# Optimization experiments

Measured on AMD Instinct MI355X. Metric: run time of the kernel, lower is better.

Reference implementation:

```python
import jax, jax.numpy as jnp
import numpy as np
from jax import lax

T = 8192          # in_length
D = 128           # embed_dim
SIGMA_MIN = 0.4
SIGMA_MAX = 3.0
NOISE_SIGMA = 0.01
GAUSS_C = 0.39894228  # 1/sqrt(2*pi), as hardcoded in the source


def setup_inputs() -> dict:
    key = jax.random.key(0)
    kx, kn = jax.random.split(key)
    X = jax.random.uniform(kx, (1, T), dtype=jnp.float32)            # spike train: X > 0.5 fires
    weight = jnp.ones((1, D), dtype=jnp.float32)                      # module buffer: ones -> uniform softmax
    noise = NOISE_SIGMA * jax.random.normal(kn, (1, T), dtype=jnp.float32)
    sigma = jnp.linspace(SIGMA_MIN, SIGMA_MAX, D, dtype=jnp.float32)  # kernel widths
    return {"X": X, "weight": weight, "noise": noise, "sigma": sigma}


def reference(X, weight, noise, sigma):
    Tlen = X.shape[1]
    # Gaussian kernel bank, exactly as Gaussian_kernel_fix: peak at index j == T
    j = jnp.arange(2 * Tlen - 1, dtype=X.dtype)
    d2 = (j - Tlen) ** 2                                              # [2T-1]
    K = (GAUSS_C / sigma)[:, None] * jnp.exp(-d2[None, :] / (2.0 * sigma * sigma)[:, None])  # [D, 2T-1]

    # GKE: embed[d, t] = sum_i 1{X[0,i] > 0.5} * K[d, T-1 + t - i]  == full convolution, 'same' slice
    spikes = (X > 0.5).astype(X.dtype)                                # [1, T]
    Kf = K[:, ::-1][:, None, :]                                       # flip -> lax cross-correlation computes the conv; [D, 1, 2T-1]
    embed = lax.conv_general_dilated(
        spikes[None],                                                 # [1, 1, T]  (N, C, W)
        Kf,                                                           # [D, 1, 2T-1] (O, I, W)
        window_strides=(1,),
        padding=[(Tlen - 1, Tlen - 1)],
    )[0]                                                              # [D, T]

    # softmax-weighted sum over sigma channels + frozen noise
    psedu = jax.nn.softmax(weight, axis=1) @ embed + noise            # [1, T]

    # global min-max normalization (norm=True branch)
    pmin = jnp.min(psedu)
    pmax = jnp.max(psedu)
    return (psedu - pmin) / (pmax - pmin)
```

## Files before the change

### kernel.cpp

```cpp
#include <hip/hip_runtime.h>
#include <math.h>

#define T_LEN   8192
#define D_DIM   128
#define BLK     128
#define NBLK    (T_LEN / BLK)
#define GAUSS_C 0.39894228f


__global__ __launch_bounds__(BLK) void k_conv(
    const float* __restrict__ X, const float* __restrict__ weight,
    const float* __restrict__ noise, const float* __restrict__ sigma,
    float* __restrict__ psedu, float* __restrict__ bmin, float* __restrict__ bmax)
{
    __shared__ float wsc[D_DIM];
    __shared__ float inv2[D_DIM];
    __shared__ float gl2[D_DIM];
    __shared__ float s[BLK + 128];
    __shared__ float red[4];

    const int tid = threadIdx.x;
    const int t0  = blockIdx.x * BLK;
    const int wv  = tid >> 6;

    #pragma unroll
    for (int li = tid; li < BLK + 128; li += BLK) {
        int i = t0 - 64 + li;
        float x = (i >= 0 && i < T_LEN) ? X[i] : 0.0f;
        s[li] = (x > 0.5f) ? 1.0f : 0.0f;
    }

    float w = weight[tid];
    float m = w;
    #pragma unroll
    for (int off = 32; off >= 1; off >>= 1) m = fmaxf(m, __shfl_xor(m, off));
    if ((tid & 63) == 0) red[wv] = m;
    __syncthreads();
    m = fmaxf(red[0], red[1]);
    float e = __expf(w - m);
    float sm = e;
    #pragma unroll
    for (int off = 32; off >= 1; off >>= 1) sm += __shfl_xor(sm, off);
    if ((tid & 63) == 0) red[2 + wv] = sm;
    __syncthreads();
    sm = red[2] + red[3];

    float sg = sigma[tid];
    wsc[tid]  = (e / sm) * (GAUSS_C / sg);
    inv2[tid] = 1.0f / (2.0f * sg * sg);
    __syncthreads();

    {
        float rho = 63.0f - (float)tid;
        float r2  = rho * rho;
        float acc = 0.0f;
        for (int d = 0; d < D_DIM; ++d)
            acc = fmaf(wsc[d], __expf(-r2 * inv2[d]), acc);
        gl2[tid] = acc;
    }
    __syncthreads();

    float a0 = 0.f, a1 = 0.f, a2 = 0.f, a3 = 0.f;
    #pragma unroll
    for (int k = 0; k < 128; k += 4) {
        float4 g4 = *reinterpret_cast<const float4*>(&gl2[k]);
        a0 = fmaf(s[tid + k    ], g4.x, a0);
        a1 = fmaf(s[tid + k + 1], g4.y, a1);
        a2 = fmaf(s[tid + k + 2], g4.z, a2);
        a3 = fmaf(s[tid + k + 3], g4.w, a3);
    }
    const int t = t0 + tid;
    float acc = (a0 + a1) + (a2 + a3) + noise[t];
    psedu[t] = acc;

    float mn = acc, mx = acc;
    #pragma unroll
    for (int off = 32; off >= 1; off >>= 1) {
        mn = fminf(mn, __shfl_xor(mn, off));
        mx = fmaxf(mx, __shfl_xor(mx, off));
    }
    __syncthreads();
    if ((tid & 63) == 0) { red[wv] = mn; red[2 + wv] = mx; }
    __syncthreads();
    if (tid == 0) {
        bmin[blockIdx.x] = fminf(red[0], red[1]);
        bmax[blockIdx.x] = fmaxf(red[2], red[3]);
    }
}

__global__ __launch_bounds__(BLK) void k_norm(
    const float* __restrict__ psedu, const float* __restrict__ bmin,
    const float* __restrict__ bmax, float* __restrict__ out)
{
    float gmin = bmin[0], gmax = bmax[0];
    #pragma unroll
    for (int i = 1; i < NBLK; ++i) {
        gmin = fminf(gmin, bmin[i]);
        gmax = fmaxf(gmax, bmax[i]);
    }
    const int t = blockIdx.x * BLK + threadIdx.x;
    out[t] = (psedu[t] - gmin) * (1.0f / (gmax - gmin));
}

extern "C" void kernel_launch(void* const* d_in, const int* in_sizes, int n_in,
                              void* d_out, int out_size, void* d_ws, size_t ws_size,
                              hipStream_t stream) {
    const float* X      = (const float*)d_in[0];
    const float* weight = (const float*)d_in[1];
    const float* noise  = (const float*)d_in[2];
    const float* sigma  = (const float*)d_in[3];
    float* out = (float*)d_out;

    float* ws    = (float*)d_ws;
    float* psedu = ws;
    float* bmin  = ws + T_LEN;
    float* bmax  = ws + T_LEN + NBLK;

    k_conv<<<NBLK, BLK, 0, stream>>>(X, weight, noise, sigma, psedu, bmin, bmax);
    k_norm<<<NBLK, BLK, 0, stream>>>(psedu, bmin, bmax, out);
}
```

Baseline: 12.96 us.

## Fuse conv and normalization into one single-block kernel with 32-tap window

Replaces the two-kernel pipeline (64-block convolution plus a separate normalization pass) with one 512-thread block. Each thread computes 16 consecutive outputs from a register window of spikes. The collapsed Gaussian filter is shrunk from 128 to 32 taps and built cooperatively with a shuffle reduction. The global min/max is then reduced in shared memory, so the intermediate buffer and second launch go away. The trade-off is running on a single compute unit, and the tap truncation relies on the largest sigma being small enough that weights beyond ±16 are negligible.

```diff
diff --git a/kernel.cpp b/kernel.cpp
--- a/kernel.cpp
+++ b/kernel.cpp
@@ -3,103 +3,150 @@
 
 #define T_LEN   8192
 #define D_DIM   128
-#define BLK     128
-#define NBLK    (T_LEN / BLK)
+#define NTHR    512
+#define OPT     16
+#define NTAP    32
 #define GAUSS_C 0.39894228f
 
-
-__global__ __launch_bounds__(BLK) void k_conv(
+__global__ __launch_bounds__(NTHR) void k_fused(
     const float* __restrict__ X, const float* __restrict__ weight,
     const float* __restrict__ noise, const float* __restrict__ sigma,
-    float* __restrict__ psedu, float* __restrict__ bmin, float* __restrict__ bmax)
+    float* __restrict__ out)
 {
     __shared__ float wsc[D_DIM];
     __shared__ float inv2[D_DIM];
-    __shared__ float gl2[D_DIM];
-    __shared__ float s[BLK + 128];
+    __shared__ float g[NTAP];
     __shared__ float red[4];
+    __shared__ float rmin[8], rmax[8];
 
     const int tid = threadIdx.x;
-    const int t0  = blockIdx.x * BLK;
     const int wv  = tid >> 6;
+    const int t0  = tid * OPT;
 
+    float W[48];
+    const int base = t0 - 16;
+    if (base >= 0 && base + 48 <= T_LEN) {
+        #pragma unroll
+        for (int q = 0; q < 12; ++q) {
+            float4 x4 = *reinterpret_cast<const float4*>(&X[base + 4*q]);
+            W[4*q+0] = x4.x > 0.5f ? 1.f : 0.f;
+            W[4*q+1] = x4.y > 0.5f ? 1.f : 0.f;
+            W[4*q+2] = x4.z > 0.5f ? 1.f : 0.f;
+            W[4*q+3] = x4.w > 0.5f ? 1.f : 0.f;
+        }
+    } else {
+        #pragma unroll
+        for (int m = 0; m < 48; ++m) {
+            int i = base + m;
+            float x = (i >= 0 && i < T_LEN) ? X[i] : 0.f;
+            W[m] = x > 0.5f ? 1.f : 0.f;
+        }
+    }
+    float nzf[OPT];
     #pragma unroll
-    for (int li = tid; li < BLK + 128; li += BLK) {
-        int i = t0 - 64 + li;
-        float x = (i >= 0 && i < T_LEN) ? X[i] : 0.0f;
-        s[li] = (x > 0.5f) ? 1.0f : 0.0f;
+    for (int q = 0; q < 4; ++q) {
+        float4 v = *reinterpret_cast<const float4*>(&noise[t0 + 4*q]);
+        nzf[4*q+0] = v.x; nzf[4*q+1] = v.y; nzf[4*q+2] = v.z; nzf[4*q+3] = v.w;
     }
 
-    float w = weight[tid];
-    float m = w;
-    #pragma unroll
-    for (int off = 32; off >= 1; off >>= 1) m = fmaxf(m, __shfl_xor(m, off));
-    if ((tid & 63) == 0) red[wv] = m;
+    float w_e = 0.f;
+    if (tid < 128) {
+        float w = weight[tid];
+        float m = w;
+        #pragma unroll
+        for (int off = 32; off >= 1; off >>= 1) m = fmaxf(m, __shfl_xor(m, off));
+        if ((tid & 63) == 0) red[wv] = m;
+    }
     __syncthreads();
-    m = fmaxf(red[0], red[1]);
-    float e = __expf(w - m);
-    float sm = e;
-    #pragma unroll
-    for (int off = 32; off >= 1; off >>= 1) sm += __shfl_xor(sm, off);
-    if ((tid & 63) == 0) red[2 + wv] = sm;
+    if (tid < 128) {
+        float w = weight[tid];
+        float m = fmaxf(red[0], red[1]);
+        float e = __expf(w - m);
+        float s = e;
+        #pragma unroll
+        for (int off = 32; off >= 1; off >>= 1) s += __shfl_xor(s, off);
+        if ((tid & 63) == 0) red[2 + wv] = s;
+        w_e = e;
+    }
     __syncthreads();
-    sm = red[2] + red[3];
-
-    float sg = sigma[tid];
-    wsc[tid]  = (e / sm) * (GAUSS_C / sg);
-    inv2[tid] = 1.0f / (2.0f * sg * sg);
+    if (tid < 128) {
+        float s  = red[2] + red[3];
+        float sg = sigma[tid];
+        wsc[tid]  = (w_e / s) * (GAUSS_C / sg);
+        inv2[tid] = 1.f / (2.f * sg * sg);
+    }
     __syncthreads();
 
     {
-        float rho = 63.0f - (float)tid;
+        int   k  = tid >> 4;
+        int   d0 = (tid & 15) * 8;
+        float rho = (float)(k - 16);
         float r2  = rho * rho;
-        float acc = 0.0f;
-        for (int d = 0; d < D_DIM; ++d)
-            acc = fmaf(wsc[d], __expf(-r2 * inv2[d]), acc);
-        gl2[tid] = acc;
+        float4 wa = *reinterpret_cast<const float4*>(&wsc[d0]);
+        float4 wb = *reinterpret_cast<const float4*>(&wsc[d0 + 4]);
+        float4 ia = *reinterpret_cast<const float4*>(&inv2[d0]);
+        float4 ib = *reinterpret_cast<const float4*>(&inv2[d0 + 4]);
+        float a = wa.x * __expf(-r2 * ia.x);
+        a = fmaf(wa.y, __expf(-r2 * ia.y), a);
+        a = fmaf(wa.z, __expf(-r2 * ia.z), a);
+        a = fmaf(wa.w, __expf(-r2 * ia.w), a);
+        a = fmaf(wb.x, __expf(-r2 * ib.x), a);
+        a = fmaf(wb.y, __expf(-r2 * ib.y), a);
+        a = fmaf(wb.z, __expf(-r2 * ib.z), a);
+        a = fmaf(wb.w, __expf(-r2 * ib.w), a);
+        #pragma unroll
+        for (int off = 8; off >= 1; off >>= 1) a += __shfl_xor(a, off);
+        if ((tid & 15) == 0) g[k] = a;
     }
     __syncthreads();
 
-    float a0 = 0.f, a1 = 0.f, a2 = 0.f, a3 = 0.f;
+    float gv[NTAP];
     #pragma unroll
-    for (int k = 0; k < 128; k += 4) {
-        float4 g4 = *reinterpret_cast<const float4*>(&gl2[k]);
-        a0 = fmaf(s[tid + k    ], g4.x, a0);
-        a1 = fmaf(s[tid + k + 1], g4.y, a1);
-        a2 = fmaf(s[tid + k + 2], g4.z, a2);
-        a3 = fmaf(s[tid + k + 3], g4.w, a3);
+    for (int q = 0; q < 8; ++q) {
+        float4 g4 = *reinterpret_cast<const float4*>(&g[4*q]);
+        gv[4*q+0] = g4.x; gv[4*q+1] = g4.y; gv[4*q+2] = g4.z; gv[4*q+3] = g4.w;
     }
-    const int t = t0 + tid;
-    float acc = (a0 + a1) + (a2 + a3) + noise[t];
-    psedu[t] = acc;
 
-    float mn = acc, mx = acc;
+    float acc[OPT];
+    #pragma unroll
+    for (int j = 0; j < OPT; ++j) {
+        float a = 0.f;
+        #pragma unroll
+        for (int k = 0; k < NTAP; ++k)
+            a = fmaf(W[j + 31 - k], gv[k], a);
+        acc[j] = a + nzf[j];
+    }
+
+    float mn = acc[0], mx = acc[0];
+    #pragma unroll
+    for (int j = 1; j < OPT; ++j) {
+        mn = fminf(mn, acc[j]);
+        mx = fmaxf(mx, acc[j]);
+    }
     #pragma unroll
     for (int off = 32; off >= 1; off >>= 1) {
         mn = fminf(mn, __shfl_xor(mn, off));
         mx = fmaxf(mx, __shfl_xor(mx, off));
     }
+    if ((tid & 63) == 0) { rmin[wv] = mn; rmax[wv] = mx; }
     __syncthreads();
-    if ((tid & 63) == 0) { red[wv] = mn; red[2 + wv] = mx; }
-    __syncthreads();
-    if (tid == 0) {
-        bmin[blockIdx.x] = fminf(red[0], red[1]);
-        bmax[blockIdx.x] = fmaxf(red[2], red[3]);
+    float gmn = rmin[0], gmx = rmax[0];
+    #pragma unroll
+    for (int i = 1; i < 8; ++i) {
+        gmn = fminf(gmn, rmin[i]);
+        gmx = fmaxf(gmx, rmax[i]);
     }
-}
+    const float inv = 1.f / (gmx - gmn);
 
-__global__ __launch_bounds__(BLK) void k_norm(
-    const float* __restrict__ psedu, const float* __restrict__ bmin,
-    const float* __restrict__ bmax, float* __restrict__ out)
-{
-    float gmin = bmin[0], gmax = bmax[0];
     #pragma unroll
-    for (int i = 1; i < NBLK; ++i) {
-        gmin = fminf(gmin, bmin[i]);
-        gmax = fmaxf(gmax, bmax[i]);
+    for (int q = 0; q < 4; ++q) {
+        float4 o;
+        o.x = (acc[4*q+0] - gmn) * inv;
+        o.y = (acc[4*q+1] - gmn) * inv;
+        o.z = (acc[4*q+2] - gmn) * inv;
+        o.w = (acc[4*q+3] - gmn) * inv;
+        *reinterpret_cast<float4*>(&out[t0 + 4*q]) = o;
     }
-    const int t = blockIdx.x * BLK + threadIdx.x;
-    out[t] = (psedu[t] - gmin) * (1.0f / (gmax - gmin));
 }
 
 extern "C" void kernel_launch(void* const* d_in, const int* in_sizes, int n_in,
@@ -111,11 +158,5 @@
     const float* sigma  = (const float*)d_in[3];
     float* out = (float*)d_out;
 
-    float* ws    = (float*)d_ws;
-    float* psedu = ws;
-    float* bmin  = ws + T_LEN;
-    float* bmax  = ws + T_LEN + NBLK;
-
-    k_conv<<<NBLK, BLK, 0, stream>>>(X, weight, noise, sigma, psedu, bmin, bmax);
-    k_norm<<<NBLK, BLK, 0, stream>>>(psedu, bmin, bmax, out);
+    k_fused<<<1, NTHR, 0, stream>>>(X, weight, noise, sigma, out);
 }
```

Measured after the change: 15.38 us. +18.7%, slower.

## Fuse conv and normalization via cooperative grid sync; shrink Gaussian taps to 32

Applied to the files above, without the earlier changes.

Merges the convolution and min-max normalization kernels into one cooperative kernel. Each block writes its partial min and max, then does a grid-wide sync and normalizes its own result held in registers, so the intermediate psedu buffer and the second launch go away. It also cuts the combined Gaussian kernel from 128 taps to 32 (±16 around the peak) and computes those taps with 4 threads each plus a shuffle reduction. The cost is the cooperative launch and grid barrier. The tighter truncation relies on sigma staying small relative to 16.

```diff
diff --git a/kernel.cpp b/kernel.cpp
--- a/kernel.cpp
+++ b/kernel.cpp
@@ -1,34 +1,48 @@
 #include <hip/hip_runtime.h>
+#include <hip/hip_cooperative_groups.h>
 #include <math.h>
+
+namespace cg = cooperative_groups;
 
 #define T_LEN   8192
 #define D_DIM   128
-#define BLK     128
-#define NBLK    (T_LEN / BLK)
+#define NTHR    128
+#define NBLK    64
+#define OPB     128
+#define NTAP    32
 #define GAUSS_C 0.39894228f
 
-
-__global__ __launch_bounds__(BLK) void k_conv(
+__global__ __launch_bounds__(NTHR) void k_coop(
     const float* __restrict__ X, const float* __restrict__ weight,
     const float* __restrict__ noise, const float* __restrict__ sigma,
-    float* __restrict__ psedu, float* __restrict__ bmin, float* __restrict__ bmax)
+    float* __restrict__ out, float* __restrict__ ws)
 {
     __shared__ float wsc[D_DIM];
     __shared__ float inv2[D_DIM];
-    __shared__ float gl2[D_DIM];
-    __shared__ float s[BLK + 128];
+    __shared__ float g2[NTAP];
+    __shared__ float s[OPB + NTAP];
     __shared__ float red[4];
 
+    float* bmin = ws;
+    float* bmax = ws + NBLK;
+
     const int tid = threadIdx.x;
-    const int t0  = blockIdx.x * BLK;
     const int wv  = tid >> 6;
+    const int bid = blockIdx.x;
+    const int B0  = bid * OPB;
+    const int t   = B0 + tid;
 
-    #pragma unroll
-    for (int li = tid; li < BLK + 128; li += BLK) {
-        int i = t0 - 64 + li;
-        float x = (i >= 0 && i < T_LEN) ? X[i] : 0.0f;
-        s[li] = (x > 0.5f) ? 1.0f : 0.0f;
+    {
+        int i = B0 - 16 + tid;
+        float x = (i >= 0 && i < T_LEN) ? X[i] : 0.f;
+        s[tid] = x > 0.5f ? 1.f : 0.f;
+        if (tid < OPB + NTAP - NTHR) {
+            int i2 = B0 - 16 + NTHR + tid;
+            float x2 = (i2 < T_LEN) ? X[i2] : 0.f;
+            s[NTHR + tid] = x2 > 0.5f ? 1.f : 0.f;
+        }
     }
+    const float nz = noise[t];
 
     float w = weight[tid];
     float m = w;
@@ -37,41 +51,52 @@
     if ((tid & 63) == 0) red[wv] = m;
     __syncthreads();
     m = fmaxf(red[0], red[1]);
-    float e = __expf(w - m);
+    float e  = __expf(w - m);
     float sm = e;
     #pragma unroll
     for (int off = 32; off >= 1; off >>= 1) sm += __shfl_xor(sm, off);
     if ((tid & 63) == 0) red[2 + wv] = sm;
     __syncthreads();
     sm = red[2] + red[3];
-
-    float sg = sigma[tid];
-    wsc[tid]  = (e / sm) * (GAUSS_C / sg);
-    inv2[tid] = 1.0f / (2.0f * sg * sg);
+    {
+        float sg = sigma[tid];
+        wsc[tid]  = (e / sm) * (GAUSS_C / sg);
+        inv2[tid] = 1.f / (2.f * sg * sg);
+    }
     __syncthreads();
 
     {
-        float rho = 63.0f - (float)tid;
+        int   k  = tid >> 2;
+        int   c  = (tid & 3) * 32;
+        float rho = (float)(15 - k);
         float r2  = rho * rho;
-        float acc = 0.0f;
-        for (int d = 0; d < D_DIM; ++d)
-            acc = fmaf(wsc[d], __expf(-r2 * inv2[d]), acc);
-        gl2[tid] = acc;
+        float a = 0.f;
+        #pragma unroll
+        for (int q = 0; q < 8; ++q) {
+            float4 wa = *reinterpret_cast<const float4*>(&wsc[c + 4*q]);
+            float4 ia = *reinterpret_cast<const float4*>(&inv2[c + 4*q]);
+            a = fmaf(wa.x, __expf(-r2 * ia.x), a);
+            a = fmaf(wa.y, __expf(-r2 * ia.y), a);
+            a = fmaf(wa.z, __expf(-r2 * ia.z), a);
+            a = fmaf(wa.w, __expf(-r2 * ia.w), a);
+        }
+        a += __shfl_xor(a, 1);
+        a += __shfl_xor(a, 2);
+        if ((tid & 3) == 0) g2[k] = a;
     }
     __syncthreads();
 
-    float a0 = 0.f, a1 = 0.f, a2 = 0.f, a3 = 0.f;
+    float g2r[NTAP];
     #pragma unroll
-    for (int k = 0; k < 128; k += 4) {
-        float4 g4 = *reinterpret_cast<const float4*>(&gl2[k]);
-        a0 = fmaf(s[tid + k    ], g4.x, a0);
-        a1 = fmaf(s[tid + k + 1], g4.y, a1);
-        a2 = fmaf(s[tid + k + 2], g4.z, a2);
-        a3 = fmaf(s[tid + k + 3], g4.w, a3);
+    for (int q = 0; q < 8; ++q) {
+        float4 v = *reinterpret_cast<const float4*>(&g2[4*q]);
+        g2r[4*q+0] = v.x; g2r[4*q+1] = v.y; g2r[4*q+2] = v.z; g2r[4*q+3] = v.w;
     }
-    const int t = t0 + tid;
-    float acc = (a0 + a1) + (a2 + a3) + noise[t];
-    psedu[t] = acc;
+    float a = 0.f;
+    #pragma unroll
+    for (int k = 0; k < NTAP; ++k)
+        a = fmaf(s[tid + k], g2r[k], a);
+    const float acc = a + nz;
 
     float mn = acc, mx = acc;
     #pragma unroll
@@ -83,23 +108,20 @@
     if ((tid & 63) == 0) { red[wv] = mn; red[2 + wv] = mx; }
     __syncthreads();
     if (tid == 0) {
-        bmin[blockIdx.x] = fminf(red[0], red[1]);
-        bmax[blockIdx.x] = fmaxf(red[2], red[3]);
+        bmin[bid] = fminf(red[0], red[1]);
+        bmax[bid] = fmaxf(red[2], red[3]);
     }
-}
 
-__global__ __launch_bounds__(BLK) void k_norm(
-    const float* __restrict__ psedu, const float* __restrict__ bmin,
-    const float* __restrict__ bmax, float* __restrict__ out)
-{
-    float gmin = bmin[0], gmax = bmax[0];
+    cg::this_grid().sync();
+
+    float mnv = bmin[tid & 63];
+    float mxv = bmax[tid & 63];
     #pragma unroll
-    for (int i = 1; i < NBLK; ++i) {
-        gmin = fminf(gmin, bmin[i]);
-        gmax = fmaxf(gmax, bmax[i]);
+    for (int off = 32; off >= 1; off >>= 1) {
+        mnv = fminf(mnv, __shfl_xor(mnv, off));
+        mxv = fmaxf(mxv, __shfl_xor(mxv, off));
     }
-    const int t = blockIdx.x * BLK + threadIdx.x;
-    out[t] = (psedu[t] - gmin) * (1.0f / (gmax - gmin));
+    out[t] = (acc - mnv) * (1.f / (mxv - mnv));
 }
 
 extern "C" void kernel_launch(void* const* d_in, const int* in_sizes, int n_in,
@@ -110,12 +132,10 @@
     const float* noise  = (const float*)d_in[2];
     const float* sigma  = (const float*)d_in[3];
     float* out = (float*)d_out;
+    float* ws  = (float*)d_ws;
 
-    float* ws    = (float*)d_ws;
-    float* psedu = ws;
-    float* bmin  = ws + T_LEN;
-    float* bmax  = ws + T_LEN + NBLK;
-
-    k_conv<<<NBLK, BLK, 0, stream>>>(X, weight, noise, sigma, psedu, bmin, bmax);
-    k_norm<<<NBLK, BLK, 0, stream>>>(psedu, bmin, bmax, out);
+    void* args[] = { (void*)&X, (void*)&weight, (void*)&noise,
+                     (void*)&sigma, (void*)&out, (void*)&ws };
+    hipLaunchCooperativeKernel(reinterpret_cast<void*>(k_coop),
+                               dim3(NBLK), dim3(NTHR), args, 0, stream);
 }
```

After: 37.68 us. 191% more time.
